# Kernel tuning notes

Measured on AMD Instinct MI355X. Metric: run time of the kernel, lower is better.

## Reference

```python
import jax, jax.numpy as jnp
import numpy as np

B, S, H, NH = 8, 1024, 1024, 16
HD = H // NH  # head dim = 64

def setup_inputs() -> dict:
    key = jax.random.key(0)
    ks = jax.random.split(key, 7)
    sc = 0.02
    return {
        "activation": jax.random.normal(ks[0], (B, S, H), jnp.float32),
        "qw": jax.random.normal(ks[1], (H, H), jnp.float32) * sc,
        "qb": jax.random.normal(ks[2], (H,), jnp.float32) * sc,
        "kw": jax.random.normal(ks[3], (H, H), jnp.float32) * sc,
        "kb": jax.random.normal(ks[4], (H,), jnp.float32) * sc,
        "vw": jax.random.normal(ks[5], (H, H), jnp.float32) * sc,
        "vb": jax.random.normal(ks[6], (H,), jnp.float32) * sc,
    }

def reference(activation, qw, qb, kw, kb, vw, vb):
    # QKV projections (torch Linear: x @ W^T + b)
    def proj(x, w, b):
        y = jnp.einsum('bsh,oh->bso', x, w) + b
        # split heads: [B,S,H] -> [B,NH,S,HD]
        return y.reshape(B, S, NH, HD).transpose(0, 2, 1, 3)
    q = proj(activation, qw, qb)
    k = proj(activation, kw, kb)
    v = proj(activation, vw, vb)
    # NOTE: source scales by 1/sqrt(hidden_dim), NOT 1/sqrt(head_dim)
    scale = 1.0 / jnp.sqrt(jnp.float32(H))
    scores = jnp.einsum('bnqd,bnkd->bnqk', q, k) * scale
    probs = jax.nn.softmax(scores, axis=-1)
    ctx = jnp.einsum('bnqk,bnkd->bnqd', probs, v)
    # merge heads: [B,NH,S,HD] -> [B,S,H]
    return ctx.transpose(0, 2, 1, 3).reshape(B, S, H)
```

## Files before the change

kernel.cpp:

```cpp
#include <hip/hip_runtime.h>
#include <cstdint>
#include <cstddef>

#define B_   8
#define S_   1024
#define H_   1024
#define NH_  16
#define HD_  64
#define M_   8192
#define N3_  3072
#define K_   1024

typedef __attribute__((ext_vector_type(8))) short bf16x8;
typedef __attribute__((ext_vector_type(4))) float f32x4;
typedef __attribute__((ext_vector_type(16))) float f32x16;
typedef __attribute__((ext_vector_type(8))) unsigned short u16x8;
typedef __attribute__((ext_vector_type(4))) unsigned u32x4;

__device__ __forceinline__ unsigned short f2bf(float f) {
  unsigned u = __builtin_bit_cast(unsigned, f);
  u += 0x7fffu + ((u >> 16) & 1u);
  return (unsigned short)(u >> 16);
}

__device__ __forceinline__ unsigned long long pack4bf(float a, float b,
                                                      float c, float d) {
  return (unsigned long long)f2bf(a)
       | ((unsigned long long)f2bf(b) << 16)
       | ((unsigned long long)f2bf(c) << 32)
       | ((unsigned long long)f2bf(d) << 48);
}

__device__ __forceinline__ unsigned cvtpk(float a, float b) {
  unsigned r;
  asm("v_cvt_pk_bf16_f32 %0, %1, %2" : "=v"(r) : "v"(a), "v"(b));
  return r;
}

__global__ void cvt_kernel(const float* __restrict__ src,
                           unsigned short* __restrict__ dst, int n) {
  const int stride = gridDim.x * blockDim.x * 8;
  for (int i = (blockIdx.x * blockDim.x + threadIdx.x) * 8; i < n; i += stride) {
    float4 a = *reinterpret_cast<const float4*>(src + i);
    float4 b = *reinterpret_cast<const float4*>(src + i + 4);
    u16x8 o;
    o[0] = f2bf(a.x); o[1] = f2bf(a.y); o[2] = f2bf(a.z); o[3] = f2bf(a.w);
    o[4] = f2bf(b.x); o[5] = f2bf(b.y); o[6] = f2bf(b.z); o[7] = f2bf(b.w);
    *reinterpret_cast<u16x8*>(dst + i) = o;
  }
}

__global__ void wcvt_kernel(const float* __restrict__ q,
                            const float* __restrict__ k,
                            const float* __restrict__ v,
                            unsigned short* __restrict__ dst) {
  const int i = (blockIdx.x * blockDim.x + threadIdx.x) * 8;
  const float* src;
  int off;
  if (i < 1048576)      { src = q; off = i; }
  else if (i < 2097152) { src = k; off = i - 1048576; }
  else                  { src = v; off = i - 2097152; }
  float4 a = *reinterpret_cast<const float4*>(src + off);
  float4 b = *reinterpret_cast<const float4*>(src + off + 4);
  u16x8 o;
  o[0] = f2bf(a.x); o[1] = f2bf(a.y); o[2] = f2bf(a.z); o[3] = f2bf(a.w);
  o[4] = f2bf(b.x); o[5] = f2bf(b.y); o[6] = f2bf(b.z); o[7] = f2bf(b.w);
  *reinterpret_cast<u16x8*>(dst + i) = o;
}

__global__ __launch_bounds__(256, 2) void qkv_gemm(
    const unsigned short* __restrict__ A,
    const unsigned short* __restrict__ Bw,
    const float* __restrict__ qb, const float* __restrict__ kb,
    const float* __restrict__ vb,
    unsigned short* __restrict__ Qh,
    unsigned short* __restrict__ Kh,
    unsigned short* __restrict__ Vth)
{
  extern __shared__ char sm[];
  const int t = threadIdx.x;
  const int lane = t & 63;
  const int wm = t >> 7, wn = (t >> 6) & 1;

  const int bid = blockIdx.x;
  const int c = bid >> 3;
  const int bm = (bid & 7) * 8 + c / 24;
  const int bn = c % 24;

  const char* Ab = (const char*)A + (size_t)bm * 128 * 2048;
  const char* Bb = (const char*)Bw + (size_t)bn * 128 * 2048;

  f32x4 acc[4][4] = {};

  #define STG(kt, buf)                                                         \
    { char* Ld = sm + (buf) * 32768;                                           \
      _Pragma("unroll")                                                        \
      for (int i = 0; i < 4; ++i) {                                            \
        const int off = (i * 256 + t) * 16;                                    \
        const int row = off >> 7;                                              \
        const int sc  = ((off >> 4) & 7) ^ (row & 7);                          \
        __builtin_amdgcn_global_load_lds(                                      \
          (const __attribute__((address_space(1))) void*)(Ab + (size_t)row * 2048 + (kt) * 128 + sc * 16), \
          (__attribute__((address_space(3))) void*)(Ld + off), 16, 0, 0);      \
        __builtin_amdgcn_global_load_lds(                                      \
          (const __attribute__((address_space(1))) void*)(Bb + (size_t)row * 2048 + (kt) * 128 + sc * 16), \
          (__attribute__((address_space(3))) void*)(Ld + 16384 + off), 16, 0, 0); \
      } }

  STG(0, 0)
  __syncthreads();

  for (int kt = 0; kt < 16; ++kt) {
    if (kt < 15) STG(kt + 1, (kt + 1) & 1)
    const char* Acur = sm + (kt & 1) * 32768;
    const char* Bcur = Acur + 16384;
    #pragma unroll
    for (int kk = 0; kk < 2; ++kk) {
      bf16x8 af[4], bf[4];
      #pragma unroll
      for (int mb = 0; mb < 4; ++mb) {
        const int row = wm * 64 + mb * 16 + (lane & 15);
        const int j   = kk * 4 + (lane >> 4);
        af[mb] = *(const bf16x8*)(Acur + row * 128 + ((j ^ (row & 7)) << 4));
      }
      #pragma unroll
      for (int nb = 0; nb < 4; ++nb) {
        const int row = wn * 64 + nb * 16 + (lane & 15);
        const int j   = kk * 4 + (lane >> 4);
        bf[nb] = *(const bf16x8*)(Bcur + row * 128 + ((j ^ (row & 7)) << 4));
      }
      __builtin_amdgcn_s_setprio(1);
      #pragma unroll
      for (int mb = 0; mb < 4; ++mb)
        #pragma unroll
        for (int nb = 0; nb < 4; ++nb)
          acc[mb][nb] = __builtin_amdgcn_mfma_f32_16x16x32_bf16(
              af[mb], bf[nb], acc[mb][nb], 0, 0, 0);
      __builtin_amdgcn_s_setprio(0);
    }
    __syncthreads();
  }

  const int tensor = bn >> 3;
  const float scl = (tensor == 0) ? 0.04508422f : 1.0f;
  const float* bias = (tensor == 0) ? qb : (tensor == 1) ? kb : vb;
  char* E = sm;
  const int bloc = bm >> 3;
  const int srow = (bm & 7) * 128;

  if (tensor < 2) {
    #pragma unroll
    for (int nb = 0; nb < 4; ++nb) {
      const int col = wn * 64 + nb * 16 + (lane & 15);
      const float bv = bias[(bn & 7) * 128 + col];
      #pragma unroll
      for (int mb = 0; mb < 4; ++mb) {
        #pragma unroll
        for (int r = 0; r < 4; ++r) {
          const int row = wm * 64 + mb * 16 + (lane >> 4) * 4 + r;
          const int byo = row * 256 + ((((col >> 3) ^ (row & 7)) << 4) | ((col & 7) << 1));
          *(unsigned short*)(E + byo) = f2bf((acc[mb][nb][r] + bv) * scl);
        }
      }
    }
    __syncthreads();
    unsigned short* dst = (tensor == 0) ? Qh : Kh;
    #pragma unroll
    for (int cch = 0; cch < 8; ++cch) {
      const int o = t * 128 + cch * 16;
      const int row = o >> 8;
      const int colb = o & 255;
      const int col = colb >> 1;
      u32x4 v = *(const u32x4*)(E + row * 256 + ((((colb >> 4) ^ (row & 7)) << 4)));
      const int sg = srow + row;
      const int nhh = (bn & 7) * 2 + (col >> 6);
      const size_t db = ((size_t)(bloc * NH_ + nhh) * S_ + sg) * 128 + (col & 63) * 2;
      *(u32x4*)((char*)dst + db) = v;
    }
  } else {
    #pragma unroll
    for (int nb = 0; nb < 4; ++nb) {
      const int col = wn * 64 + nb * 16 + (lane & 15);
      const float bv = bias[(bn & 7) * 128 + col];
      #pragma unroll
      for (int mb = 0; mb < 4; ++mb) {
        const int row0 = wm * 64 + mb * 16 + (lane >> 4) * 4;
        unsigned long long w = pack4bf(acc[mb][nb][0] + bv, acc[mb][nb][1] + bv,
                                       acc[mb][nb][2] + bv, acc[mb][nb][3] + bv);
        const int byo = col * 256 + ((((row0 >> 3) ^ (col & 7)) << 4) | ((row0 & 7) << 1));
        *(unsigned long long*)(E + byo) = w;
      }
    }
    __syncthreads();
    #pragma unroll
    for (int cch = 0; cch < 8; ++cch) {
      const int o = t * 128 + cch * 16;
      const int col = o >> 8;
      const int rowb = o & 255;
      const int row0 = rowb >> 1;
      u32x4 v = *(const u32x4*)(E + col * 256 + ((((rowb >> 4) ^ (col & 7)) << 4)));
      const int sg0 = srow + row0;
      const int nhh = (bn & 7) * 2 + (col >> 6);
      const size_t db = (size_t)(bloc * NH_ + nhh) * 131072 +
                        (size_t)(sg0 >> 6) * 8192 + (col & 63) * 128 + (sg0 & 63) * 2;
      *(u32x4*)((char*)Vth + db) = v;
    }
  }
}

__device__ __forceinline__ bf16x8 mk_frag(const f32x16& s, const int base) {
  unsigned a0 = cvtpk(s[base + 0], s[base + 1]);
  unsigned a1 = cvtpk(s[base + 2], s[base + 3]);
  unsigned b0 = cvtpk(s[base + 4], s[base + 5]);
  unsigned b1 = cvtpk(s[base + 6], s[base + 7]);
  asm("v_permlane32_swap_b32 %0, %1" : "+v"(a0), "+v"(b0));
  asm("v_permlane32_swap_b32 %0, %1" : "+v"(a1), "+v"(b1));
  u32x4 u = {a0, a1, b0, b1};
  return __builtin_bit_cast(bf16x8, u);
}

__global__ __launch_bounds__(256, 3) void attn_kernel(
    const unsigned short* __restrict__ Qh,
    const unsigned short* __restrict__ Kh,
    const unsigned short* __restrict__ Vth,
    float* __restrict__ Out)
{
  __shared__ char smx[2][16384];
  const int t = threadIdx.x;
  const int lane = t & 63;
  const int wave = t >> 6;
  const int l31 = lane & 31;
  const int hi = lane >> 5;
  const int hw = blockIdx.x;
  const int xcd = hw & 7;
  const int qt = (hw >> 3) & 7;
  const int bh = (hw >> 6) * 8 + xcd;
  const int b = bh >> 4, nh = bh & 15;

  const unsigned short* Qp = Qh + (size_t)bh * (S_ * HD_);
  const char* Kp = (const char*)Kh + (size_t)bh * 131072;
  const char* Vp = (const char*)Vth + (size_t)bh * 131072;
  const int q0 = qt * 128 + wave * 32;

  bf16x8 bq[4];
  #pragma unroll
  for (int st = 0; st < 4; ++st)
    bq[st] = *reinterpret_cast<const bf16x8*>(
        Qp + (size_t)(q0 + l31) * HD_ + st * 16 + hi * 8);

  const int soff0 = wave * 1024 + lane * 16;
  #define STAGE_TILE(dstbase, srcbase)                                            \
    _Pragma("unroll")                                                             \
    for (int j = 0; j < 2; ++j) {                                                 \
      const int off = j * 4096 + soff0;                                           \
      const int row = off >> 7;                                                   \
      const int sc  = ((off >> 4) & 7) ^ (row & 7);                               \
      __builtin_amdgcn_global_load_lds(                                           \
          (const __attribute__((address_space(1))) void*)((srcbase) + row * 128 + sc * 16), \
          (__attribute__((address_space(3))) void*)((dstbase) + off), 16, 0, 0);  \
    }

  STAGE_TILE(&smx[0][0],    Kp)
  STAGE_TILE(&smx[0][8192], Vp)
  __syncthreads();

  f32x16 o0 = {}, o1 = {};
  float lsum = 0.f;
  const int swr = l31 & 7;

  for (int kt = 0; kt < 16; ++kt) {
    const int cur = kt & 1;
    if (kt < 15) {
      STAGE_TILE(&smx[cur ^ 1][0],    Kp + (kt + 1) * 8192)
      STAGE_TILE(&smx[cur ^ 1][8192], Vp + (kt + 1) * 8192)
    }
    const char* Kb = &smx[cur][0];
    const char* Vb = &smx[cur][8192];

    f32x16 s0 = {}, s1 = {};
    #pragma unroll
    for (int st = 0; st < 4; ++st) {
      const int c = ((st * 2 + hi) ^ swr) << 4;
      bf16x8 ka = *reinterpret_cast<const bf16x8*>(Kb + l31 * 128 + c);
      bf16x8 kc = *reinterpret_cast<const bf16x8*>(Kb + (l31 + 32) * 128 + c);
      s0 = __builtin_amdgcn_mfma_f32_32x32x16_bf16(ka, bq[st], s0, 0, 0, 0);
      s1 = __builtin_amdgcn_mfma_f32_32x32x16_bf16(kc, bq[st], s1, 0, 0, 0);
    }

    bf16x8 va[4];
    #pragma unroll
    for (int ks = 0; ks < 2; ++ks) {
      const int c = ((ks * 2 + hi) ^ swr) << 4;
      va[ks * 2]     = *reinterpret_cast<const bf16x8*>(Vb + l31 * 128 + c);
      va[ks * 2 + 1] = *reinterpret_cast<const bf16x8*>(Vb + (l31 + 32) * 128 + c);
    }
    #pragma unroll
    for (int r = 0; r < 16; ++r) {
      s0[r] = __builtin_amdgcn_exp2f(s0[r]);
      lsum += s0[r];
    }
    bf16x8 f0 = mk_frag(s0, 0);
    bf16x8 f1 = mk_frag(s0, 8);
    o0 = __builtin_amdgcn_mfma_f32_32x32x16_bf16(f0, va[0], o0, 0, 0, 0);
    o1 = __builtin_amdgcn_mfma_f32_32x32x16_bf16(f0, va[1], o1, 0, 0, 0);
    o0 = __builtin_amdgcn_mfma_f32_32x32x16_bf16(f1, va[2], o0, 0, 0, 0);
    o1 = __builtin_amdgcn_mfma_f32_32x32x16_bf16(f1, va[3], o1, 0, 0, 0);

    #pragma unroll
    for (int ks = 0; ks < 2; ++ks) {
      const int c = (((ks + 2) * 2 + hi) ^ swr) << 4;
      va[ks * 2]     = *reinterpret_cast<const bf16x8*>(Vb + l31 * 128 + c);
      va[ks * 2 + 1] = *reinterpret_cast<const bf16x8*>(Vb + (l31 + 32) * 128 + c);
    }
    #pragma unroll
    for (int r = 0; r < 16; ++r) {
      s1[r] = __builtin_amdgcn_exp2f(s1[r]);
      lsum += s1[r];
    }
    bf16x8 f2 = mk_frag(s1, 0);
    bf16x8 f3 = mk_frag(s1, 8);
    o0 = __builtin_amdgcn_mfma_f32_32x32x16_bf16(f2, va[0], o0, 0, 0, 0);
    o1 = __builtin_amdgcn_mfma_f32_32x32x16_bf16(f2, va[1], o1, 0, 0, 0);
    o0 = __builtin_amdgcn_mfma_f32_32x32x16_bf16(f3, va[2], o0, 0, 0, 0);
    o1 = __builtin_amdgcn_mfma_f32_32x32x16_bf16(f3, va[3], o1, 0, 0, 0);

    __syncthreads();
  }

  const float ltot = lsum + __shfl_xor(lsum, 32);
  const float inv = 1.0f / ltot;
  #pragma unroll
  for (int r = 0; r < 16; ++r) {
    const int crow = (r & 3) + 8 * (r >> 2) + 4 * hi;
    const float invq = __shfl(inv, crow);
    float* op = Out + ((size_t)(b * S_ + q0 + crow)) * H_ + nh * HD_ + l31;
    op[0]  = o0[r] * invq;
    op[32] = o1[r] * invq;
  }
}

extern "C" void kernel_launch(void* const* d_in, const int* in_sizes, int n_in,
                              void* d_out, int out_size, void* d_ws, size_t ws_size,
                              hipStream_t stream) {
  const float* act = (const float*)d_in[0];
  const float* qw  = (const float*)d_in[1];
  const float* qb  = (const float*)d_in[2];
  const float* kw  = (const float*)d_in[3];
  const float* kb  = (const float*)d_in[4];
  const float* vw  = (const float*)d_in[5];
  const float* vb  = (const float*)d_in[6];

  char* ws = (char*)d_ws;
  unsigned short* actb = (unsigned short*)ws;
  unsigned short* wb   = (unsigned short*)(ws + 16777216);
  unsigned short* Qh   = (unsigned short*)(ws + 23068672);
  unsigned short* Kh   = Qh + 8388608;
  unsigned short* Vth  = Kh + 8388608;

  cvt_kernel<<<4096, 256, 0, stream>>>(act, actb, M_ * K_);
  wcvt_kernel<<<1536, 256, 0, stream>>>(qw, kw, vw, wb);

  hipFuncSetAttribute((const void*)qkv_gemm,
                      hipFuncAttributeMaxDynamicSharedMemorySize, 65536);
  qkv_gemm<<<1536, 256, 65536, stream>>>(actb, wb, qb, kb, vb, Qh, Kh, Vth);

  attn_kernel<<<1024, 256, 0, stream>>>(Qh, Kh, Vth, (float*)d_out);
}
```

Measured before the change: 123.5 us.

## Switch QKV GEMM to triple-buffered BK=32 pipeline with explicit vmcnt waits

The QKV projection GEMM now uses a K-tile of 32 instead of 64 and three LDS buffers instead of two, with a matching XOR swizzle for 64-byte rows. Loads run two stages ahead, and each step waits with s_waitcnt vmcnt(4) plus a raw s_barrier instead of a full __syncthreads. Shared memory per block drops to 48KB and launch bounds rise to 3 blocks per CU, aiming for more occupancy and better overlap of global-to-LDS loads with MFMA work. The cost is twice as many loop iterations and barriers. The epilogue reuses LDS, and correctness depends on the hand-written wait counts matching the outstanding loads.

```diff
diff --git a/kernel.cpp b/kernel.cpp
--- a/kernel.cpp
+++ b/kernel.cpp
@@ -68,7 +68,7 @@
   *reinterpret_cast<u16x8*>(dst + i) = o;
 }
 
-__global__ __launch_bounds__(256, 2) void qkv_gemm(
+__global__ __launch_bounds__(256, 3) void qkv_gemm(
     const unsigned short* __restrict__ A,
     const unsigned short* __restrict__ Bw,
     const float* __restrict__ qb, const float* __restrict__ kb,
@@ -93,53 +93,59 @@
   f32x4 acc[4][4] = {};
 
   #define STG(kt, buf)                                                         \
-    { char* Ld = sm + (buf) * 32768;                                           \
+    { char* Ld = sm + (buf) * 16384;                                           \
       _Pragma("unroll")                                                        \
-      for (int i = 0; i < 4; ++i) {                                            \
-        const int off = (i * 256 + t) * 16;                                    \
-        const int row = off >> 7;                                              \
-        const int sc  = ((off >> 4) & 7) ^ (row & 7);                          \
+      for (int j = 0; j < 2; ++j) {                                            \
+        const int off = j * 4096 + t * 16;                                     \
+        const int row = off >> 6;                                              \
+        const int sc  = (((off >> 4) & 3) ^ ((row >> 1) & 3));                 \
         __builtin_amdgcn_global_load_lds(                                      \
-          (const __attribute__((address_space(1))) void*)(Ab + (size_t)row * 2048 + (kt) * 128 + sc * 16), \
+          (const __attribute__((address_space(1))) void*)(Ab + (size_t)row * 2048 + (kt) * 64 + sc * 16), \
           (__attribute__((address_space(3))) void*)(Ld + off), 16, 0, 0);      \
         __builtin_amdgcn_global_load_lds(                                      \
-          (const __attribute__((address_space(1))) void*)(Bb + (size_t)row * 2048 + (kt) * 128 + sc * 16), \
-          (__attribute__((address_space(3))) void*)(Ld + 16384 + off), 16, 0, 0); \
+          (const __attribute__((address_space(1))) void*)(Bb + (size_t)row * 2048 + (kt) * 64 + sc * 16), \
+          (__attribute__((address_space(3))) void*)(Ld + 8192 + off), 16, 0, 0); \
       } }
 
+  #define VM4 asm volatile("s_waitcnt vmcnt(4)" ::: "memory")
+  #define VM0 asm volatile("s_waitcnt vmcnt(0)" ::: "memory")
+  #define BARR asm volatile("s_barrier" ::: "memory")
+
   STG(0, 0)
+  STG(1, 1)
+  VM4;
+  BARR;
+
+  for (int kt = 0; kt < 32; ++kt) {
+    if (kt < 30) STG(kt + 2, (kt + 2) % 3)
+    const char* Abuf = sm + (kt % 3) * 16384;
+    const char* Bbuf = Abuf + 8192;
+    bf16x8 af[4], bf[4];
+    #pragma unroll
+    for (int mb = 0; mb < 4; ++mb) {
+      const int row = wm * 64 + mb * 16 + (lane & 15);
+      af[mb] = *(const bf16x8*)(Abuf + row * 64 +
+                (((lane >> 4) ^ ((row >> 1) & 3)) << 4));
+    }
+    #pragma unroll
+    for (int nb = 0; nb < 4; ++nb) {
+      const int row = wn * 64 + nb * 16 + (lane & 15);
+      bf[nb] = *(const bf16x8*)(Bbuf + row * 64 +
+                (((lane >> 4) ^ ((row >> 1) & 3)) << 4));
+    }
+    __builtin_amdgcn_s_setprio(1);
+    #pragma unroll
+    for (int mb = 0; mb < 4; ++mb)
+      #pragma unroll
+      for (int nb = 0; nb < 4; ++nb)
+        acc[mb][nb] = __builtin_amdgcn_mfma_f32_16x16x32_bf16(
+            af[mb], bf[nb], acc[mb][nb], 0, 0, 0);
+    __builtin_amdgcn_s_setprio(0);
+    if (kt < 30)       VM4;
+    else if (kt == 30) VM0;
+    if (kt < 31) BARR;
+  }
   __syncthreads();
-
-  for (int kt = 0; kt < 16; ++kt) {
-    if (kt < 15) STG(kt + 1, (kt + 1) & 1)
-    const char* Acur = sm + (kt & 1) * 32768;
-    const char* Bcur = Acur + 16384;
-    #pragma unroll
-    for (int kk = 0; kk < 2; ++kk) {
-      bf16x8 af[4], bf[4];
-      #pragma unroll
-      for (int mb = 0; mb < 4; ++mb) {
-        const int row = wm * 64 + mb * 16 + (lane & 15);
-        const int j   = kk * 4 + (lane >> 4);
-        af[mb] = *(const bf16x8*)(Acur + row * 128 + ((j ^ (row & 7)) << 4));
-      }
-      #pragma unroll
-      for (int nb = 0; nb < 4; ++nb) {
-        const int row = wn * 64 + nb * 16 + (lane & 15);
-        const int j   = kk * 4 + (lane >> 4);
-        bf[nb] = *(const bf16x8*)(Bcur + row * 128 + ((j ^ (row & 7)) << 4));
-      }
-      __builtin_amdgcn_s_setprio(1);
-      #pragma unroll
-      for (int mb = 0; mb < 4; ++mb)
-        #pragma unroll
-        for (int nb = 0; nb < 4; ++nb)
-          acc[mb][nb] = __builtin_amdgcn_mfma_f32_16x16x32_bf16(
-              af[mb], bf[nb], acc[mb][nb], 0, 0, 0);
-      __builtin_amdgcn_s_setprio(0);
-    }
-    __syncthreads();
-  }
 
   const int tensor = bn >> 3;
   const float scl = (tensor == 0) ? 0.04508422f : 1.0f;
@@ -361,8 +367,8 @@
   wcvt_kernel<<<1536, 256, 0, stream>>>(qw, kw, vw, wb);
 
   hipFuncSetAttribute((const void*)qkv_gemm,
-                      hipFuncAttributeMaxDynamicSharedMemorySize, 65536);
-  qkv_gemm<<<1536, 256, 65536, stream>>>(actb, wb, qb, kb, vb, Qh, Kh, Vth);
+                      hipFuncAttributeMaxDynamicSharedMemorySize, 49152);
+  qkv_gemm<<<1536, 256, 49152, stream>>>(actb, wb, qb, kb, vb, Qh, Kh, Vth);
 
   attn_kernel<<<1024, 256, 0, stream>>>(Qh, Kh, Vth, (float*)d_out);
 }
```

After: 130.1 us. 5.4% more time.
